# Kernel optimization log

Hardware: AMD Instinct MI355X
Metric: run time of the kernel (lower is better)

## Reference

```python
import jax, jax.numpy as jnp
import numpy as np

MARGIN = 0.3
ANCHOR = 0.5
EPS = 1e-8  # torch F.cosine_similarity default eps


def _cosine(a, b):
    # a: [N, D], b: [D] -> [N]
    num = a @ b
    den = jnp.maximum(jnp.linalg.norm(a, axis=-1) * jnp.linalg.norm(b), EPS)
    return num / den


def setup_inputs() -> dict:
    key = jax.random.key(0)
    k1, k2, k3, k4 = jax.random.split(key, 4)
    N, D = 8192, 1024
    return {
        "q_emb": jax.random.normal(k1, (D,), dtype=jnp.float32),
        "d_embs": jax.random.normal(k2, (N, D), dtype=jnp.float32),
        "c_emb": jax.random.normal(k3, (D,), dtype=jnp.float32),
        "rates": jax.random.uniform(k4, (N,), dtype=jnp.float32),
    }


def reference(q_emb, d_embs, c_emb, rates):
    # cosine similarity of each distractor vs question / correct answer
    s_q = _cosine(d_embs, q_emb)          # [N]
    _s_c = _cosine(d_embs, c_emb)         # [N] computed in original, never used
    quality = jnp.abs(rates - ANCHOR)     # [N]

    # Vectorized form of the nested i,j loop:
    # pair (i, j) contributes relu(margin + s_q[j] - s_q[i]) iff quality[i] > quality[j]
    mask = quality[:, None] > quality[None, :]              # [N, N]; diagonal is False
    pair_loss = jax.nn.relu(MARGIN + s_q[None, :] - s_q[:, None])  # [N, N]
    total = jnp.sum(jnp.where(mask, pair_loss, jnp.float32(0.0)))
    n_pairs = jnp.sum(mask)
    return total / jnp.maximum(n_pairs, 1).astype(total.dtype)
```

## Files before the change

### kernel.cpp

```cpp
#include <hip/hip_runtime.h>

#define MARGIN 0.3f
#define ANCHOR 0.5f
#define EPS    1e-8f
#define BJ     256
#define NSLOT  32

typedef unsigned long long ull;


__global__ __launch_bounds__(256) void sq_kernel(
        const float* __restrict__ q, const float* __restrict__ d,
        const float* __restrict__ rates,
        float* __restrict__ sq, float* __restrict__ qual,
        char* __restrict__ acc, int N, int D) {
    int tid = threadIdx.x;
    if (blockIdx.x == 0) {
        if (tid < NSLOT)              *(double*)  (acc + (size_t)tid * 64)               = 0.0;
        else if (tid < 2 * NSLOT)     *(unsigned*)(acc + 2048 + (size_t)(tid - 32) * 64) = 0u;
        else if (tid < 3 * NSLOT)     *(unsigned*)(acc + 4096 + (size_t)(tid - 64) * 64) = 0u;
        else if (tid == 3 * NSLOT)    *(unsigned*)(acc + 6144)                           = 0u;
    }
    int wave = (blockIdx.x * blockDim.x + tid) >> 6;
    int lane = tid & 63;
    if (wave >= N) return;
    const float* row = d + (size_t)wave * (size_t)D;

    float dot = 0.f, dn = 0.f, qn = 0.f;
    for (int it = lane * 4; it < D; it += 256) {
        float4 dv = *(const float4*)(row + it);
        float4 qv = *(const float4*)(q + it);
        dot += dv.x * qv.x + dv.y * qv.y + dv.z * qv.z + dv.w * qv.w;
        dn  += dv.x * dv.x + dv.y * dv.y + dv.z * dv.z + dv.w * dv.w;
        qn  += qv.x * qv.x + qv.y * qv.y + qv.z * qv.z + qv.w * qv.w;
    }
    #pragma unroll
    for (int off = 32; off >= 1; off >>= 1) {
        dot += __shfl_xor(dot, off);
        dn  += __shfl_xor(dn,  off);
        qn  += __shfl_xor(qn,  off);
    }
    if (lane == 0) {
        float den = fmaxf(sqrtf(dn) * sqrtf(qn), EPS);
        sq[wave]   = dot / den;
        qual[wave] = fabsf(rates[wave] - ANCHOR);
    }
}

__global__ __launch_bounds__(256) void pair_kernel(
        const float* __restrict__ sq, const float* __restrict__ qual,
        int N, char* __restrict__ acc, float* __restrict__ out, unsigned nblocks) {
    __shared__ float2   tile[BJ];
    __shared__ double   bsum[4];
    __shared__ unsigned bcnt[4];

    int tid = threadIdx.x;
    int i   = blockIdx.x * blockDim.x + tid;
    int j0  = blockIdx.y * BJ;

    if (tid < BJ) {
        int j = j0 + tid;
        tile[tid] = make_float2(j < N ? sq[j]   : 0.f,
                                j < N ? qual[j] : 1e30f);
    }
    __syncthreads();

    float my_sq = (i < N) ? sq[i]   : 0.f;
    float my_q  = (i < N) ? qual[i] : -1.f;
    float a     = MARGIN - my_sq;

    float    sum = 0.f;
    unsigned c   = 0;
    #pragma unroll 8
    for (int j = 0; j < BJ; ++j) {
        float2 t = tile[j];
        bool  m = my_q > t.y;
        float v = fmaxf(a + t.x, 0.f);
        sum += m ? v : 0.f;
        c   += (unsigned)__popcll(__ballot(m));
    }

    #pragma unroll
    for (int off = 32; off >= 1; off >>= 1)
        sum += __shfl_xor(sum, off);

    int w = tid >> 6;
    if ((tid & 63) == 0) { bsum[w] = (double)sum; bcnt[w] = c; }
    __syncthreads();

    if (tid >= 64) return;

    unsigned last = 0;
    if (tid == 0) {
        double   bs = bsum[0] + bsum[1] + bsum[2] + bsum[3];
        unsigned bc = bcnt[0] + bcnt[1] + bcnt[2] + bcnt[3];
        unsigned bid = blockIdx.y * gridDim.x + blockIdx.x;
        unsigned s   = bid & (NSLOT - 1);

        double   old  = atomicAdd((double*)  (acc + (size_t)s * 64), bs);
        unsigned oldc = atomicAdd((unsigned*)(acc + 2048 + (size_t)s * 64), bc);
        asm volatile("" :: "v"(__double2hiint(old)), "v"(__double2loint(old)), "v"(oldc));

        unsigned gsz = (nblocks > s) ? ((nblocks - 1u - s) / NSLOT + 1u) : 0u;
        unsigned pa  = atomicAdd((unsigned*)(acc + 4096 + (size_t)s * 64), 1u);
        if (pa == gsz - 1u) {
            asm volatile("" :: "v"(pa));
            unsigned nslots = (nblocks < NSLOT) ? nblocks : NSLOT;
            unsigned pm = atomicAdd((unsigned*)(acc + 6144), 1u);
            last = (pm == nslots - 1u) ? 1u : 0u;
        }
    }
    last = __shfl(last, 0);
    if (last) {
        double s = 0.0; ull c2 = 0ull;
        if (tid < NSLOT) {
            s  = atomicAdd((double*)  (acc + (size_t)tid * 64), 0.0);
            c2 = (ull)atomicAdd((unsigned*)(acc + 2048 + (size_t)tid * 64), 0u);
        }
        #pragma unroll
        for (int off = 16; off >= 1; off >>= 1) {
            s  += __shfl_xor(s,  off);
            c2 += __shfl_xor(c2, off);
        }
        if (tid == 0) {
            if (c2 < 1ull) c2 = 1ull;
            out[0] = (float)(s / (double)c2);
        }
    }
}

extern "C" void kernel_launch(void* const* d_in, const int* in_sizes, int n_in,
                              void* d_out, int out_size, void* d_ws, size_t ws_size,
                              hipStream_t stream) {
    const float* q_emb  = (const float*)d_in[0];
    const float* d_embs = (const float*)d_in[1];
    const float* rates  = (const float*)d_in[3];

    int D = in_sizes[0];
    int N = in_sizes[3];

    char*  acc  = (char*)d_ws;
    float* sq   = (float*)(acc + 8192);
    float* qual = sq + N;
    float* out  = (float*)d_out;

    int rows_per_block = 256 / 64;
    sq_kernel<<<(N + rows_per_block - 1) / rows_per_block, 256, 0, stream>>>(
        q_emb, d_embs, rates, sq, qual, acc, N, D);

    dim3 grid((N + 255) / 256, (N + BJ - 1) / BJ);
    pair_kernel<<<grid, 256, 0, stream>>>(sq, qual, N, acc, out,
                                          grid.x * grid.y);
}
```

Measured before the change: 22.61 us.

## Interleave sq/quality into float2 and stream j-tile via scalar loads

The cosine kernel now writes the similarity and quality as one interleaved float2 array. The pair kernel drops the LDS tile and its __syncthreads, and reads the wave-uniform j entries through inline-asm s_load_dwordx16 into scalar registers, 16 pairs at a time. Each lane's compare and relu then use SGPR operands instead of LDS reads. The risk is a full lgkmcnt wait per 16-element chunk that may stall, plus inline asm whose SGPR alignment and constraints must be right.

```diff
diff --git a/kernel.cpp b/kernel.cpp
--- a/kernel.cpp
+++ b/kernel.cpp
@@ -7,12 +7,12 @@
 #define NSLOT  32
 
 typedef unsigned long long ull;
+typedef __attribute__((ext_vector_type(16))) float f16v;
 
 
 __global__ __launch_bounds__(256) void sq_kernel(
         const float* __restrict__ q, const float* __restrict__ d,
-        const float* __restrict__ rates,
-        float* __restrict__ sq, float* __restrict__ qual,
+        const float* __restrict__ rates, float2* __restrict__ pairs,
         char* __restrict__ acc, int N, int D) {
     int tid = threadIdx.x;
     if (blockIdx.x == 0) {
@@ -42,15 +42,13 @@
     }
     if (lane == 0) {
         float den = fmaxf(sqrtf(dn) * sqrtf(qn), EPS);
-        sq[wave]   = dot / den;
-        qual[wave] = fabsf(rates[wave] - ANCHOR);
+        pairs[wave] = make_float2(dot / den, fabsf(rates[wave] - ANCHOR));
     }
 }
 
 __global__ __launch_bounds__(256) void pair_kernel(
-        const float* __restrict__ sq, const float* __restrict__ qual,
+        const float2* __restrict__ pairs,
         int N, char* __restrict__ acc, float* __restrict__ out, unsigned nblocks) {
-    __shared__ float2   tile[BJ];
     __shared__ double   bsum[4];
     __shared__ unsigned bcnt[4];
 
@@ -58,25 +56,48 @@
     int i   = blockIdx.x * blockDim.x + tid;
     int j0  = blockIdx.y * BJ;
 
-    if (tid < BJ) {
-        int j = j0 + tid;
-        tile[tid] = make_float2(j < N ? sq[j]   : 0.f,
-                                j < N ? qual[j] : 1e30f);
-    }
-    __syncthreads();
-
-    float my_sq = (i < N) ? sq[i]   : 0.f;
-    float my_q  = (i < N) ? qual[i] : -1.f;
-    float a     = MARGIN - my_sq;
+    float my_sq = 0.f, my_q = -1.f;
+    if (i < N) { float2 p = pairs[i]; my_sq = p.x; my_q = p.y; }
+    float a = MARGIN - my_sq;
 
     float    sum = 0.f;
     unsigned c   = 0;
-    #pragma unroll 8
-    for (int j = 0; j < BJ; ++j) {
-        float2 t = tile[j];
-        bool  m = my_q > t.y;
-        float v = fmaxf(a + t.x, 0.f);
-        sum += m ? v : 0.f;
+    int jmax = N - j0; if (jmax > BJ) jmax = BJ;
+
+    int g = 0;
+    for (; g + 16 <= jmax; g += 16) {
+        const float2* p = pairs + j0 + g;
+        f16v A, B;
+        asm volatile(
+            "s_load_dwordx16 %0, %2, 0x0\n\t"
+            "s_load_dwordx16 %1, %2, 0x40\n\t"
+            "s_waitcnt lgkmcnt(0)"
+            : "=&s"(A), "=&s"(B)
+            : "s"(p));
+        #pragma unroll
+        for (int k = 0; k < 8; ++k) {
+            float sj = A[2 * k], qj = A[2 * k + 1];
+            bool  m = my_q > qj;
+            float t = a + sj;
+            float z = m ? t : 0.f;
+            sum += fmaxf(z, 0.f);
+            c   += (unsigned)__popcll(__ballot(m));
+        }
+        #pragma unroll
+        for (int k = 0; k < 8; ++k) {
+            float sj = B[2 * k], qj = B[2 * k + 1];
+            bool  m = my_q > qj;
+            float t = a + sj;
+            float z = m ? t : 0.f;
+            sum += fmaxf(z, 0.f);
+            c   += (unsigned)__popcll(__ballot(m));
+        }
+    }
+    for (; g < jmax; ++g) {
+        float2 pj = pairs[j0 + g];
+        bool  m = my_q > pj.y;
+        float t = a + pj.x;
+        sum += m ? fmaxf(t, 0.f) : 0.f;
         c   += (unsigned)__popcll(__ballot(m));
     }
 
@@ -139,16 +160,15 @@
     int D = in_sizes[0];
     int N = in_sizes[3];
 
-    char*  acc  = (char*)d_ws;
-    float* sq   = (float*)(acc + 8192);
-    float* qual = sq + N;
-    float* out  = (float*)d_out;
+    char*   acc   = (char*)d_ws;
+    float2* pairs = (float2*)(acc + 8192);
+    float*  out   = (float*)d_out;
 
     int rows_per_block = 256 / 64;
     sq_kernel<<<(N + rows_per_block - 1) / rows_per_block, 256, 0, stream>>>(
-        q_emb, d_embs, rates, sq, qual, acc, N, D);
+        q_emb, d_embs, rates, pairs, acc, N, D);
 
     dim3 grid((N + 255) / 256, (N + BJ - 1) / BJ);
-    pair_kernel<<<grid, 256, 0, stream>>>(sq, qual, N, acc, out,
+    pair_kernel<<<grid, 256, 0, stream>>>(pairs, N, acc, out,
                                           grid.x * grid.y);
 }
```

After: 24.39 us. 7.9% more time.

## Replace last-block atomic finalize with separate finalize kernel and pack sq/quality

Applied to the files above, without the earlier changes.

Removes the arrival-counter scheme that detected the last pair block and moves the final reduction into a separate one-wave finalize kernel. The per-row similarity and quality values are now stored interleaved as float2, so each load gathers both. BJ is halved, which doubles the number of pair blocks while shortening each block's inner loop. In exchange the change adds a third kernel launch, and there are twice as many atomics into the accumulation slots.

```diff
diff --git a/kernel.cpp b/kernel.cpp
--- a/kernel.cpp
+++ b/kernel.cpp
@@ -3,7 +3,7 @@
 #define MARGIN 0.3f
 #define ANCHOR 0.5f
 #define EPS    1e-8f
-#define BJ     256
+#define BJ     128
 #define NSLOT  32
 
 typedef unsigned long long ull;
@@ -11,15 +11,12 @@
 
 __global__ __launch_bounds__(256) void sq_kernel(
         const float* __restrict__ q, const float* __restrict__ d,
-        const float* __restrict__ rates,
-        float* __restrict__ sq, float* __restrict__ qual,
+        const float* __restrict__ rates, float2* __restrict__ pairs,
         char* __restrict__ acc, int N, int D) {
     int tid = threadIdx.x;
     if (blockIdx.x == 0) {
-        if (tid < NSLOT)              *(double*)  (acc + (size_t)tid * 64)               = 0.0;
-        else if (tid < 2 * NSLOT)     *(unsigned*)(acc + 2048 + (size_t)(tid - 32) * 64) = 0u;
-        else if (tid < 3 * NSLOT)     *(unsigned*)(acc + 4096 + (size_t)(tid - 64) * 64) = 0u;
-        else if (tid == 3 * NSLOT)    *(unsigned*)(acc + 6144)                           = 0u;
+        if (tid < NSLOT)          *(double*)  (acc + (size_t)tid * 64)               = 0.0;
+        else if (tid < 2 * NSLOT) *(unsigned*)(acc + 2048 + (size_t)(tid - 32) * 64) = 0u;
     }
     int wave = (blockIdx.x * blockDim.x + tid) >> 6;
     int lane = tid & 63;
@@ -42,14 +39,13 @@
     }
     if (lane == 0) {
         float den = fmaxf(sqrtf(dn) * sqrtf(qn), EPS);
-        sq[wave]   = dot / den;
-        qual[wave] = fabsf(rates[wave] - ANCHOR);
+        pairs[wave] = make_float2(dot / den, fabsf(rates[wave] - ANCHOR));
     }
 }
 
 __global__ __launch_bounds__(256) void pair_kernel(
-        const float* __restrict__ sq, const float* __restrict__ qual,
-        int N, char* __restrict__ acc, float* __restrict__ out, unsigned nblocks) {
+        const float2* __restrict__ pairs,
+        int N, char* __restrict__ acc) {
     __shared__ float2   tile[BJ];
     __shared__ double   bsum[4];
     __shared__ unsigned bcnt[4];
@@ -60,14 +56,14 @@
 
     if (tid < BJ) {
         int j = j0 + tid;
-        tile[tid] = make_float2(j < N ? sq[j]   : 0.f,
-                                j < N ? qual[j] : 1e30f);
+        float2 p = (j < N) ? pairs[j] : make_float2(0.f, 1e30f);
+        tile[tid] = p;
     }
     __syncthreads();
 
-    float my_sq = (i < N) ? sq[i]   : 0.f;
-    float my_q  = (i < N) ? qual[i] : -1.f;
-    float a     = MARGIN - my_sq;
+    float my_sq = 0.f, my_q = -1.f;
+    if (i < N) { float2 p = pairs[i]; my_sq = p.x; my_q = p.y; }
+    float a = MARGIN - my_sq;
 
     float    sum = 0.f;
     unsigned c   = 0;
@@ -88,44 +84,32 @@
     if ((tid & 63) == 0) { bsum[w] = (double)sum; bcnt[w] = c; }
     __syncthreads();
 
-    if (tid >= 64) return;
-
-    unsigned last = 0;
     if (tid == 0) {
         double   bs = bsum[0] + bsum[1] + bsum[2] + bsum[3];
         unsigned bc = bcnt[0] + bcnt[1] + bcnt[2] + bcnt[3];
         unsigned bid = blockIdx.y * gridDim.x + blockIdx.x;
         unsigned s   = bid & (NSLOT - 1);
+        atomicAdd((double*)  (acc + (size_t)s * 64), bs);
+        atomicAdd((unsigned*)(acc + 2048 + (size_t)s * 64), bc);
+    }
+}
 
-        double   old  = atomicAdd((double*)  (acc + (size_t)s * 64), bs);
-        unsigned oldc = atomicAdd((unsigned*)(acc + 2048 + (size_t)s * 64), bc);
-        asm volatile("" :: "v"(__double2hiint(old)), "v"(__double2loint(old)), "v"(oldc));
-
-        unsigned gsz = (nblocks > s) ? ((nblocks - 1u - s) / NSLOT + 1u) : 0u;
-        unsigned pa  = atomicAdd((unsigned*)(acc + 4096 + (size_t)s * 64), 1u);
-        if (pa == gsz - 1u) {
-            asm volatile("" :: "v"(pa));
-            unsigned nslots = (nblocks < NSLOT) ? nblocks : NSLOT;
-            unsigned pm = atomicAdd((unsigned*)(acc + 6144), 1u);
-            last = (pm == nslots - 1u) ? 1u : 0u;
-        }
+__global__ __launch_bounds__(64) void finalize_kernel(
+        char* __restrict__ acc, float* __restrict__ out) {
+    int lane = threadIdx.x;
+    double s = 0.0; ull c = 0ull;
+    if (lane < NSLOT) {
+        s = atomicAdd((double*)  (acc + (size_t)lane * 64), 0.0);
+        c = (ull)atomicAdd((unsigned*)(acc + 2048 + (size_t)lane * 64), 0u);
     }
-    last = __shfl(last, 0);
-    if (last) {
-        double s = 0.0; ull c2 = 0ull;
-        if (tid < NSLOT) {
-            s  = atomicAdd((double*)  (acc + (size_t)tid * 64), 0.0);
-            c2 = (ull)atomicAdd((unsigned*)(acc + 2048 + (size_t)tid * 64), 0u);
-        }
-        #pragma unroll
-        for (int off = 16; off >= 1; off >>= 1) {
-            s  += __shfl_xor(s,  off);
-            c2 += __shfl_xor(c2, off);
-        }
-        if (tid == 0) {
-            if (c2 < 1ull) c2 = 1ull;
-            out[0] = (float)(s / (double)c2);
-        }
+    #pragma unroll
+    for (int off = 16; off >= 1; off >>= 1) {
+        s += __shfl_xor(s, off);
+        c += __shfl_xor(c, off);
+    }
+    if (lane == 0) {
+        if (c < 1ull) c = 1ull;
+        out[0] = (float)(s / (double)c);
     }
 }
 
@@ -139,16 +123,16 @@
     int D = in_sizes[0];
     int N = in_sizes[3];
 
-    char*  acc  = (char*)d_ws;
-    float* sq   = (float*)(acc + 8192);
-    float* qual = sq + N;
-    float* out  = (float*)d_out;
+    char*   acc   = (char*)d_ws;
+    float2* pairs = (float2*)(acc + 8192);
+    float*  out   = (float*)d_out;
 
     int rows_per_block = 256 / 64;
     sq_kernel<<<(N + rows_per_block - 1) / rows_per_block, 256, 0, stream>>>(
-        q_emb, d_embs, rates, sq, qual, acc, N, D);
+        q_emb, d_embs, rates, pairs, acc, N, D);
 
     dim3 grid((N + 255) / 256, (N + BJ - 1) / BJ);
-    pair_kernel<<<grid, 256, 0, stream>>>(sq, qual, N, acc, out,
-                                          grid.x * grid.y);
+    pair_kernel<<<grid, 256, 0, stream>>>(pairs, N, acc);
+
+    finalize_kernel<<<1, 64, 0, stream>>>(acc, out);
 }
```

Measured after the change: 20.85 us. 7.8% less time.
